# Kernel tuning notes

Measured on AMD Instinct MI355X. Metric: run time of the kernel, lower is better.

Reference implementation:

```python
import jax, jax.numpy as jnp
import numpy as np
from jax.scipy.special import logsumexp

B, T, D = 16, 512, 768
S, H, O = 4, 48, 48
EMISS_W = 0.5  # args.emiss_nn_weight


def setup_inputs() -> dict:
    key = jax.random.key(0)
    ks = jax.random.split(key, 6)
    emb = jax.random.normal(ks[0], (B, T, D), jnp.float32)
    # obs must be valid per-source distributions over n_obs (log is taken)
    obs = jax.nn.softmax(2.0 * jax.random.normal(ks[1], (B, T, S, O), jnp.float32), axis=-1)
    # default prior init: priors = 0.001, priors[0] = 1, param = log(priors)
    p = jnp.full((H,), 0.001, jnp.float32).at[0].set(1.0)
    state_priors = jnp.log(p)
    unnorm_trans = jax.random.normal(ks[2], (H, H), jnp.float32)
    unnorm_emiss = jnp.zeros((S, H, O), jnp.float32)
    # xavier_uniform with relu gain for the per-source emission Linears
    bound = np.sqrt(2.0) * np.sqrt(6.0 / (D + H * O))
    W_emiss = jax.random.uniform(ks[3], (S, H * O, D), jnp.float32, -bound, bound)
    b_emiss = jnp.zeros((S, H * O), jnp.float32)
    seq_lengths = jax.random.randint(ks[4], (B,), T // 2, T + 1).astype(jnp.int32)
    seq_lengths = seq_lengths.at[0].set(T)  # max length == T
    return dict(emb=emb, obs=obs, state_priors=state_priors, unnorm_trans=unnorm_trans,
                unnorm_emiss=unnorm_emiss, W_emiss=W_emiss, b_emiss=b_emiss,
                seq_lengths=seq_lengths)


def _lognorm(x):
    return x - logsumexp(x, axis=-1, keepdims=True)


def reference(emb, obs, state_priors, unnorm_trans, unnorm_emiss, W_emiss, b_emiss, seq_lengths):
    lp = jax.nn.log_softmax(state_priors)                 # [H]
    log_trans = jax.nn.log_softmax(unnorm_trans, axis=-1)  # [H,H] (constant over b,t)
    emiss = jax.nn.softmax(unnorm_emiss, axis=-1)          # [S,H,O]

    # neural emissions: per-source Linear(d_emb -> H*O), softmax over O
    logits = jnp.einsum('btd,sod->btso', emb, W_emiss) + b_emiss  # [B,T,S,H*O]
    nn_emiss = jax.nn.softmax(logits.reshape(B, T, S, H, O), axis=-1)
    # (nn_trans is computed by NeuralModule in the original but discarded)

    log_emiss = jnp.log((1.0 - EMISS_W) * emiss[None, None] + EMISS_W * nn_emiss)  # [B,T,S,H,O]
    # log_matmul over obs axis, then sum over sources -> [B,T,H]
    lep = logsumexp(log_emiss + jnp.log(obs)[:, :, :, None, :], axis=-1).sum(axis=2)

    # forward recursion (normalized each step)
    a0 = _lognorm(lp + lep[:, 0])                          # [B,H]

    def fstep(a_prev, lep_t):
        a = _lognorm(lep_t + logsumexp(a_prev[:, :, None] + log_trans[None], axis=1))
        return a, a

    _, alphas = jax.lax.scan(fstep, a0, jnp.swapaxes(lep[:, 1:], 0, 1))
    log_alpha = jnp.concatenate([a0[:, None], jnp.swapaxes(alphas, 0, 1)], axis=1)  # [B,T,H]

    # backward recursion: beta[t] = logsumexp_j(trans[i,j] + lep[t,j] + beta[t+1,j])
    bT = jnp.zeros((B, H), lep.dtype)

    def bstep(b_next, lep_t):
        b = logsumexp(log_trans[None] + (lep_t + b_next)[:, None, :], axis=2)
        return b, b

    _, betas = jax.lax.scan(bstep, bT, jnp.swapaxes(lep[:, :T - 1], 0, 1), reverse=True)
    log_beta = jnp.concatenate([jnp.swapaxes(betas, 0, 1), bT[:, None]], axis=1)  # [B,T,H]
    # per-example roll by (length - T) along time, as in the original
    log_beta = jax.vmap(lambda b, s: jnp.roll(b, s, axis=0))(log_beta, seq_lengths - T)

    log_gamma = _lognorm(log_alpha + log_beta)             # [B,T,H]

    # xi_t = trans + alpha[t-1] (outer-sum) (lep[t] + beta[t]),  t = 1..T-1
    xi = (log_trans[None, None]
          + log_alpha[:, :-1, :, None]
          + (lep[:, 1:] + log_beta[:, 1:])[:, :, None, :])  # [B,T-1,H,H]
    xi = xi - logsumexp(xi, axis=(-2, -1), keepdims=True)

    log_prior = jnp.mean(jnp.sum(jnp.exp(log_gamma[:, 0]) * lp, axis=-1))

    tran_terms = jnp.sum(jnp.exp(xi) * log_trans[None, None], axis=(-2, -1))  # [B,T-1]
    mask_tr = (jnp.arange(T - 1)[None] < (seq_lengths - 1)[:, None]).astype(lep.dtype)
    log_tran = jnp.mean(jnp.sum(tran_terms * mask_tr, axis=1))

    emis_terms = jnp.sum(jnp.exp(log_gamma) * lep, axis=-1)  # [B,T]
    mask_em = (jnp.arange(T)[None] < seq_lengths[:, None]).astype(lep.dtype)
    log_emis = jnp.mean(jnp.sum(emis_terms * mask_em, axis=1))

    return log_prior + log_tran + log_emis
```

## Files before the change

### kernel.cpp

```cpp
#include <hip/hip_runtime.h>
#include <math.h>

namespace {

constexpr int Bn = 16, Tn = 512, Dn = 768, Sn = 4, Hn = 48, On = 48;
constexpr int Mn = Bn * Tn;
constexpr int Gn = Sn * Hn;
constexpr int Nn = Gn * On;
constexpr float EMISS_W = 0.5f;

constexpr size_t OFF_LP   = 0;
constexpr size_t OFF_LT   = 64;
constexpr size_t OFF_PT   = OFF_LT + Hn*Hn;
constexpr size_t OFF_EM   = OFF_PT + Hn*Hn;
constexpr size_t OFF_LEPP = OFF_EM + (size_t)Sn*Hn*On;
constexpr size_t OFF_LA   = OFF_LEPP + (size_t)Mn*Gn;
constexpr size_t OFF_LB   = OFF_LA + (size_t)Mn*Hn;
constexpr size_t OFF_RED  = OFF_LB + (size_t)Mn*Hn;
constexpr size_t FLOATS_END = OFF_RED + (size_t)Mn;

typedef __attribute__((ext_vector_type(8))) short short8;
typedef __attribute__((ext_vector_type(4))) float f32x4;

__device__ inline float waveSum(float v){
#pragma unroll
  for (int o = 32; o; o >>= 1) v += __shfl_xor(v, o);
  return v;
}

__device__ inline unsigned short f2bf(float f){
  unsigned int u = __float_as_uint(f);
  u += 0x7FFFu + ((u >> 16) & 1u);
  return (unsigned short)(u >> 16);
}

__device__ inline void gload_lds16(const void* g, void* l){
  __builtin_amdgcn_global_load_lds(
      (const __attribute__((address_space(1))) void*)g,
      (__attribute__((address_space(3))) void*)l, 16, 0, 0);
}

__global__ void convprep_kernel(const float* __restrict__ srcA, unsigned short* __restrict__ dstA,
                                int n4a,
                                const float* __restrict__ srcB, unsigned short* __restrict__ dstB,
                                int n4b,
                                const float* __restrict__ sp, const float* __restrict__ ut,
                                const float* __restrict__ ue, float* __restrict__ ws,
                                int nconv){
  const int tid = threadIdx.x;
  if ((int)blockIdx.x == nconv){
    float m = -INFINITY;
    for (int h = 0; h < Hn; ++h) m = fmaxf(m, sp[h]);
    float s = 0.f;
    for (int h = 0; h < Hn; ++h) s += __expf(sp[h] - m);
    float lse = m + __logf(s);
    if (tid < Hn) ws[OFF_LP + tid] = sp[tid] - lse;
    if (tid < Hn){
      const float* row = ut + tid * Hn;
      float mm = -INFINITY;
      for (int j = 0; j < Hn; ++j) mm = fmaxf(mm, row[j]);
      float ss = 0.f;
      for (int j = 0; j < Hn; ++j) ss += __expf(row[j] - mm);
      float l = mm + __logf(ss);
      for (int j = 0; j < Hn; ++j){
        float v = row[j] - l;
        ws[OFF_LT + tid*Hn + j] = v;
        ws[OFF_PT + tid*Hn + j] = __expf(v);
      }
    }
    for (int r = tid; r < Sn*Hn; r += blockDim.x){
      const float* row = ue + (size_t)r * On;
      float mm = -INFINITY;
      for (int o = 0; o < On; ++o) mm = fmaxf(mm, row[o]);
      float ss = 0.f;
      for (int o = 0; o < On; ++o) ss += __expf(row[o] - mm);
      float inv = 1.f/ss;
      for (int o = 0; o < On; ++o) ws[OFF_EM + (size_t)r*On + o] = __expf(row[o]-mm)*inv;
    }
    return;
  }
  int i = blockIdx.x * blockDim.x + tid;
  const float* s2; unsigned short* d; int k;
  if (i < n4a){ s2 = srcA; d = dstA; k = i; }
  else { k = i - n4a; if (k >= n4b) return; s2 = srcB; d = dstB; }
  float4 v = ((const float4*)s2)[k];
  ushort4 r;
  r.x = f2bf(v.x); r.y = f2bf(v.y); r.z = f2bf(v.z); r.w = f2bf(v.w);
  ((ushort4*)d)[k] = r;
}

constexpr int MT = 128, NT2 = 96, KT = 64;

__global__ __launch_bounds__(256) void gemm_lep_kernel(
    const unsigned short* __restrict__ embB, const unsigned short* __restrict__ WB,
    const float* __restrict__ bm, const float* __restrict__ obs,
    float* __restrict__ ws){
  __shared__ __align__(16) char smem[128*97*4];
  __shared__ float bias_s[96], em_s[96];
  const int tid = threadIdx.x, lane = tid & 63, w = tid >> 6;
  const int m0 = blockIdx.x * MT;
  const int N0 = blockIdx.y * NT2;
  if (tid < 96){
    bias_s[tid] = bm[N0 + tid];
    em_s[tid]   = ws[OFF_EM + N0 + tid];
  }
  const int wm = w & 1, wn = w >> 1;
  const int lm = lane & 15, q = lane >> 4;
  const int key = lm & 7;
  const int srow = lane >> 3, spc = lane & 7;

  f32x4 acc[4][3];
#pragma unroll
  for (int i=0;i<4;++i)
#pragma unroll
    for (int j=0;j<3;++j) acc[i][j] = (f32x4){0.f,0.f,0.f,0.f};

  for (int kc = 0; kc < Dn; kc += KT){
    __syncthreads();
#pragma unroll
    for (int i=0;i<4;++i){
      int idx = w*4 + i;
      int row = idx*8 + srow;
      int lc  = spc ^ (row & 7);
      gload_lds16(embB + (size_t)(m0+row)*Dn + kc + lc*8, smem + idx*1024);
    }
#pragma unroll
    for (int i=0;i<3;++i){
      int idx = w*3 + i;
      int row = idx*8 + srow;
      int lc  = spc ^ (row & 7);
      gload_lds16(WB + (size_t)(N0+row)*Dn + kc + lc*8, smem + 16384 + idx*1024);
    }
    __syncthreads();
#pragma unroll
    for (int s = 0; s < 2; ++s){
      short8 af[4], bf[3];
#pragma unroll
      for (int i=0;i<4;++i){
        int row = wm*64 + i*16 + lm;
        af[i] = *(const short8*)(smem + row*128 + (((s*4+q) ^ key) * 16));
      }
#pragma unroll
      for (int j=0;j<3;++j){
        int row = wn*48 + j*16 + lm;
        bf[j] = *(const short8*)(smem + 16384 + row*128 + (((s*4+q) ^ key) * 16));
      }
#pragma unroll
      for (int i=0;i<4;++i)
#pragma unroll
        for (int j=0;j<3;++j)
          acc[i][j] = __builtin_amdgcn_mfma_f32_16x16x32_bf16(af[i], bf[j], acc[i][j], 0, 0, 0);
    }
  }
  __syncthreads();
  float* C = (float*)smem;
#pragma unroll
  for (int i=0;i<4;++i)
#pragma unroll
    for (int j=0;j<3;++j)
#pragma unroll
      for (int r=0;r<4;++r){
        int mrow = wm*64 + i*16 + q*4 + r;
        int ncol = wn*48 + j*16 + lm;
        C[mrow*97 + ncol] = acc[i][j][r];
      }
  __syncthreads();
  {
    const int row = tid >> 1, half = tid & 1;
    const int m = m0 + row;
    const int g = N0/48 + half;
    const int s2 = g / Hn;
    const float* crow = C + row*97 + half*48;
    const float* ob   = obs + ((size_t)m*Sn + s2)*On;
    const float* bi   = bias_s + half*48;
    const float* em   = em_s + half*48;
    float Z=0.f, pd=0.f, eo=0.f;
#pragma unroll
    for (int o=0;o<On;++o){
      float e = __expf(crow[o] + bi[o]);
      float obv = ob[o];
      Z += e;
      pd = fmaf(e, obv, pd);
      eo = fmaf(em[o], obv, eo);
    }
    float val = __logf((1.f-EMISS_W)*eo + EMISS_W*(pd/Z));
    ws[OFF_LEPP + (size_t)m*Gn + g] = val;
  }
}

constexpr int FBW = 24;
constexpr int FBL = 16;

__global__ __launch_bounds__(64) void fb_kernel(float* __restrict__ ws){
  __shared__ __align__(16) float ldsE[(FBW+FBL)*48];
  __shared__ __align__(16) float ring[2][64];
  const int lane = threadIdx.x;
  const int c    = blockIdx.x;
  const int b    = blockIdx.y;
  const bool fwd = blockIdx.z == 0;
  const bool act = lane < Hn;
  const int t0 = c*FBL, te = t0 + FBL - 1;

  float pt[Hn];
#pragma unroll
  for (int i = 0; i < Hn; ++i)
    pt[i] = act ? (fwd ? ws[OFF_PT + i*Hn + lane] : ws[OFF_PT + lane*Hn + i]) : 0.f;

  int row_lo, nrows, sA, sZ;
  bool exact;
  if (fwd){
    sA = t0 - FBW;
    exact = (sA < 1);
    row_lo = exact ? 0 : sA;
    if (exact) sA = 1;
    sZ = te;
    nrows = te - row_lo + 1;
  } else {
    int th = te + 1 + FBW;
    exact = (th > Tn - 2);
    sA = exact ? Tn - 2 : th - 1;
    sZ = t0;
    row_lo = t0;
    nrows = sA - t0 + 1;
  }

  {
    const float* src = ws + OFF_LEPP + ((size_t)b*Tn + row_lo)*Gn;
    int n4 = nrows * (Hn/4);
    for (int i = lane; i < n4; i += 64){
      int r = i / (Hn/4), h4 = i - r*(Hn/4);
      const float* p = src + (size_t)r*Gn + h4*4;
      float4 a = *(const float4*)(p);
      float4 b2 = *(const float4*)(p + Hn);
      float4 c2 = *(const float4*)(p + 2*Hn);
      float4 d2 = *(const float4*)(p + 3*Hn);
      float4 e;
      e.x = __expf(a.x + b2.x + c2.x + d2.x);
      e.y = __expf(a.y + b2.y + c2.y + d2.y);
      e.z = __expf(a.z + b2.z + c2.z + d2.z);
      e.w = __expf(a.w + b2.w + c2.w + d2.w);
      ((float4*)ldsE)[i] = e;
    }
  }
  __syncthreads();

  if (fwd){
    const size_t laF = OFF_LA + (size_t)b * Tn * Hn;
    float v;
    if (exact){
      v = act ? __expf(ws[OFF_LP + lane]) * ldsE[lane] : 0.f;
      if (c == 0 && act) ws[laF + lane] = v;
    } else {
      v = act ? 1.f : 0.f;
    }
    if (act) ring[0][lane] = v;
    __syncthreads();
    int cur = 0;
    for (int t = sA; t <= sZ; ++t){
      float S = waveSum(v);
      const float* rp = ring[cur];
      float s0=0.f,s1=0.f,s2=0.f,s3=0.f;
#pragma unroll
      for (int i = 0; i < Hn; i += 4){
        float4 a = *(const float4*)(rp + i);
        s0 = fmaf(a.x, pt[i+0], s0); s1 = fmaf(a.y, pt[i+1], s1);
        s2 = fmaf(a.z, pt[i+2], s2); s3 = fmaf(a.w, pt[i+3], s3);
      }
      float sd = (s0+s1)+(s2+s3);
      float e = act ? ldsE[(t - row_lo)*Hn + lane] : 0.f;
      float vn = act ? e * sd * (1.f/S) : 0.f;
      cur ^= 1;
      if (act) ring[cur][lane] = vn;
      __syncthreads();
      if (act && t >= t0) ws[laF + (size_t)t*Hn + lane] = vn;
      v = vn;
    }
  } else {
    const size_t lbF = OFF_LB + (size_t)b * Tn * Hn;
    float v = act ? 1.f : 0.f;
    if (exact && c == (Tn/FBL - 1) && act) ws[lbF + (size_t)(Tn-1)*Hn + lane] = 1.f;
    int cur = 0;
    for (int t = sA; t >= sZ; --t){
      float e = act ? ldsE[(t - row_lo)*Hn + lane] : 0.f;
      float wv = e * v;
      if (act) ring[cur][lane] = wv;
      float S = waveSum(wv);
      __syncthreads();
      const float* rp = ring[cur];
      float s0=0.f,s1=0.f,s2=0.f,s3=0.f;
#pragma unroll
      for (int j = 0; j < Hn; j += 4){
        float4 a = *(const float4*)(rp + j);
        s0 = fmaf(a.x, pt[j+0], s0); s1 = fmaf(a.y, pt[j+1], s1);
        s2 = fmaf(a.z, pt[j+2], s2); s3 = fmaf(a.w, pt[j+3], s3);
      }
      float vn = act ? ((s0+s1)+(s2+s3)) * (1.f/S) : 0.f;
      cur ^= 1;
      if (act && t <= te) ws[lbF + (size_t)t*Hn + lane] = vn;
      v = vn;
    }
  }
}

__global__ __launch_bounds__(256) void gamma_xi_kernel(
    const float* __restrict__ ws_c, float* __restrict__ ws,
    const int* __restrict__ seq_len){
  __shared__ float y_s[Hn], lap_s[Hn];
  __shared__ float red[8];
  const int tid = threadIdx.x;
  const int bid = blockIdx.x;
  const int b = bid >> 9, t = bid & (Tn-1);
  const int len = seq_len[b];
  int tb = t + (Tn - len); if (tb >= Tn) tb -= Tn;
  const size_t bt = (size_t)b*Tn + t;
  float lep = 0.f;
  if (tid < Hn){
    const float* lpp = ws_c + OFF_LEPP + bt*Gn + tid;
    lep = lpp[0] + lpp[Hn] + lpp[2*Hn] + lpp[3*Hn];
    float lb  = ws_c[OFF_LB + ((size_t)b*Tn + tb)*Hn + tid];
    y_s[tid] = __expf(lep) * lb;
    if (t >= 1) lap_s[tid] = ws_c[OFF_LA + (bt-1)*Hn + tid];
  }
  float emis_term = 0.f, prior_term = 0.f;
  if (tid < 64){
    int h = (tid < Hn) ? tid : 0;
    float la  = ws_c[OFF_LA + bt*Hn + h];
    float lb  = ws_c[OFF_LB + ((size_t)b*Tn + tb)*Hn + h];
    float lp  = ws_c[OFF_LP + h];
    float wgt = (tid < Hn) ? la*lb : 0.f;
    float Z = waveSum(wgt);
    float inv = 1.f / Z;
    emis_term  = waveSum(wgt * lep) * inv;
    prior_term = waveSum(wgt * lp) * inv;
  }
  __syncthreads();
  float tran_term = 0.f;
  if (t >= 1){
    float se = 0.f, st = 0.f;
#pragma unroll
    for (int k=0;k<9;++k){
      int e = tid + k*256;
      int i = e / Hn, j = e - i*Hn;
      float e2 = ws_c[OFF_PT + e] * lap_s[i] * y_s[j];
      se += e2;
      st = fmaf(e2, ws_c[OFF_LT + e], st);
    }
    se = waveSum(se);
    st = waveSum(st);
    const int wid = tid >> 6;
    if ((tid & 63) == 0){ red[wid] = se; red[4+wid] = st; }
    __syncthreads();
    if (tid == 0){
      float SE = red[0]+red[1]+red[2]+red[3];
      float ST = red[4]+red[5]+red[6]+red[7];
      tran_term = ST / SE;
    }
  }
  if (tid == 0){
    float tot = 0.f;
    if (t < len)            tot += emis_term;
    if (t == 0)             tot += prior_term;
    if (t >= 1 && t < len)  tot += tran_term;
    ws[OFF_RED + bid] = tot;
  }
}

__global__ __launch_bounds__(256) void sum_kernel(const float* __restrict__ ws,
                                                  float* __restrict__ out){
  __shared__ float red[4];
  const int tid = threadIdx.x;
  float s = 0.f;
  for (int i = tid; i < Mn; i += 256) s += ws[OFF_RED + i];
  s = waveSum(s);
  if ((tid & 63) == 0) red[tid >> 6] = s;
  __syncthreads();
  if (tid == 0) out[0] = (red[0]+red[1]+red[2]+red[3]) * (1.f / Bn);
}

}

extern "C" void kernel_launch(void* const* d_in, const int* in_sizes, int n_in,
                              void* d_out, int out_size, void* d_ws, size_t ws_size,
                              hipStream_t stream){
  const float* emb = (const float*)d_in[0];
  const float* obs = (const float*)d_in[1];
  const float* sp  = (const float*)d_in[2];
  const float* ut  = (const float*)d_in[3];
  const float* ue  = (const float*)d_in[4];
  const float* Wm  = (const float*)d_in[5];
  const float* bm  = (const float*)d_in[6];
  const int*   sl  = (const int*)d_in[7];
  float* ws  = (float*)d_ws;
  float* out = (float*)d_out;
  (void)in_sizes; (void)n_in; (void)ws_size; (void)out_size;

  unsigned short* embB = (unsigned short*)(ws + FLOATS_END);
  unsigned short* WB   = embB + (size_t)Mn * Dn;

  const int n4a = Mn*Dn/4, n4b = Nn*Dn/4;
  const int nconv = (n4a + n4b + 255)/256;
  convprep_kernel<<<nconv + 1, 256, 0, stream>>>(emb, embB, n4a, Wm, WB, n4b,
                                                 sp, ut, ue, ws, nconv);
  gemm_lep_kernel<<<dim3(Mn/MT, Nn/NT2), 256, 0, stream>>>(embB, WB, bm, obs, ws);
  fb_kernel<<<dim3(Tn/FBL, Bn, 2), 64, 0, stream>>>(ws);
  gamma_xi_kernel<<<Bn*Tn, 256, 0, stream>>>(ws, ws, sl);
  sum_kernel<<<1, 256, 0, stream>>>(ws, out);
}
```

Before: 293.4 us.

## Enlarge GEMM tiles, double-buffer LDS with interleaved prefetch, swizzle block order

The emission GEMM moves from 128x96 tiles with 256 threads to 256x192 tiles with 512 threads. It double-buffers the K slices in LDS, issuing next-slice global-to-LDS loads between the MFMA phases, and uses explicit barriers, waitcnt and setprio to overlap loads with compute. The block index is remapped so neighbouring blocks share operand tiles in cache. The epilogue runs in two halves through the reused LDS. Together these target GEMM memory latency and reuse, at the cost of higher register and LDS pressure, fewer blocks, and fragile hand-written synchronization.

```diff
diff --git a/kernel.cpp b/kernel.cpp
--- a/kernel.cpp
+++ b/kernel.cpp
@@ -89,18 +89,26 @@
   ((ushort4*)d)[k] = r;
 }
 
-constexpr int MT = 128, NT2 = 96, KT = 64;
-
-__global__ __launch_bounds__(256) void gemm_lep_kernel(
+constexpr int BM = 256, BN = 192, BK = 64;
+constexpr int NKT = Dn / BK;
+
+#define GEMM_BAR()  asm volatile("s_barrier" ::: "memory")
+#define GEMM_LGKM() do { asm volatile("s_waitcnt lgkmcnt(0)" ::: "memory"); \
+                         __builtin_amdgcn_sched_barrier(0); } while (0)
+
+__global__ __launch_bounds__(512, 2) void gemm_lep_kernel(
     const unsigned short* __restrict__ embB, const unsigned short* __restrict__ WB,
     const float* __restrict__ bm, const float* __restrict__ obs,
     float* __restrict__ ws){
-  __shared__ __align__(16) char smem[128*97*4];
-  __shared__ float bias_s[96], em_s[96];
+  __shared__ __align__(16) char smem[114688];
+  __shared__ float bias_s[192], em_s[192];
   const int tid = threadIdx.x, lane = tid & 63, w = tid >> 6;
-  const int m0 = blockIdx.x * MT;
-  const int N0 = blockIdx.y * NT2;
-  if (tid < 96){
+  const int bid = blockIdx.y * (Mn/BM) + blockIdx.x;
+  const int swz = (bid & 7) * 192 + (bid >> 3);
+  const int m0 = (swz & 31) * BM;
+  const int by = swz >> 5;
+  const int N0 = by * BN;
+  if (tid < 192){
     bias_s[tid] = bm[N0 + tid];
     em_s[tid]   = ws[OFF_EM + N0 + tid];
   }
@@ -108,83 +116,144 @@
   const int lm = lane & 15, q = lane >> 4;
   const int key = lm & 7;
   const int srow = lane >> 3, spc = lane & 7;
-
-  f32x4 acc[4][3];
-#pragma unroll
-  for (int i=0;i<4;++i)
-#pragma unroll
-    for (int j=0;j<3;++j) acc[i][j] = (f32x4){0.f,0.f,0.f,0.f};
-
-  for (int kc = 0; kc < Dn; kc += KT){
+  const int aoff0 = (q ^ key) << 4;
+  const int aoff1 = ((4 + q) ^ key) << 4;
+
+  f32x4 acc[8][3];
+#pragma unroll
+  for (int i = 0; i < 8; ++i)
+#pragma unroll
+    for (int j = 0; j < 3; ++j) acc[i][j] = (f32x4){0.f,0.f,0.f,0.f};
+
+  auto stageA = [&](int kt, int i){
+    const int idx = w*4 + i;
+    const int row = idx*8 + srow;
+    const int lc  = spc ^ (row & 7);
+    gload_lds16(embB + (size_t)(m0+row)*Dn + kt*BK + lc*8,
+                smem + ((kt & 1) << 15) + idx*1024);
+  };
+  auto stageB = [&](int kt, int i){
+    const int idx = w*3 + i;
+    const int row = idx*8 + srow;
+    const int lc  = spc ^ (row & 7);
+    gload_lds16(WB + (size_t)(N0+row)*Dn + kt*BK + lc*8,
+                smem + 65536 + (kt & 1)*24576 + idx*1024);
+  };
+
+#pragma unroll
+  for (int i = 0; i < 4; ++i) stageA(0, i);
+#pragma unroll
+  for (int i = 0; i < 3; ++i) stageB(0, i);
+  asm volatile("s_waitcnt vmcnt(0)" ::: "memory");
+  GEMM_BAR();
+
+  for (int kt = 0; kt < NKT; ++kt){
+    const char* Ab = smem + ((kt & 1) << 15);
+    const char* Bb = smem + 65536 + (kt & 1)*24576;
+    const int pf = kt + 1;
+    const bool dopf = pf < NKT;
+    short8 af[4], bf[3];
+
+#pragma unroll
+    for (int j = 0; j < 3; ++j)
+      bf[j] = *(const short8*)(Bb + (wn*48 + j*16 + lm)*128 + aoff0);
+#pragma unroll
+    for (int i = 0; i < 4; ++i)
+      af[i] = *(const short8*)(Ab + (wm*128 + i*16 + lm)*128 + aoff0);
+    if (dopf){ stageA(pf, 0); stageA(pf, 1); stageB(pf, 0); }
+    GEMM_BAR(); GEMM_LGKM();
+    __builtin_amdgcn_s_setprio(1);
+#pragma unroll
+    for (int i = 0; i < 4; ++i)
+#pragma unroll
+      for (int j = 0; j < 3; ++j)
+        acc[i][j] = __builtin_amdgcn_mfma_f32_16x16x32_bf16(af[i], bf[j], acc[i][j], 0, 0, 0);
+    __builtin_amdgcn_s_setprio(0);
+    GEMM_BAR();
+
+#pragma unroll
+    for (int i = 0; i < 4; ++i)
+      af[i] = *(const short8*)(Ab + (wm*128 + (4+i)*16 + lm)*128 + aoff0);
+    if (dopf){ stageA(pf, 2); stageA(pf, 3); stageB(pf, 1); }
+    GEMM_BAR(); GEMM_LGKM();
+    __builtin_amdgcn_s_setprio(1);
+#pragma unroll
+    for (int i = 0; i < 4; ++i)
+#pragma unroll
+      for (int j = 0; j < 3; ++j)
+        acc[4+i][j] = __builtin_amdgcn_mfma_f32_16x16x32_bf16(af[i], bf[j], acc[4+i][j], 0, 0, 0);
+    __builtin_amdgcn_s_setprio(0);
+    GEMM_BAR();
+
+#pragma unroll
+    for (int j = 0; j < 3; ++j)
+      bf[j] = *(const short8*)(Bb + (wn*48 + j*16 + lm)*128 + aoff1);
+#pragma unroll
+    for (int i = 0; i < 4; ++i)
+      af[i] = *(const short8*)(Ab + (wm*128 + i*16 + lm)*128 + aoff1);
+    if (dopf){ stageB(pf, 2); }
+    GEMM_BAR(); GEMM_LGKM();
+    __builtin_amdgcn_s_setprio(1);
+#pragma unroll
+    for (int i = 0; i < 4; ++i)
+#pragma unroll
+      for (int j = 0; j < 3; ++j)
+        acc[i][j] = __builtin_amdgcn_mfma_f32_16x16x32_bf16(af[i], bf[j], acc[i][j], 0, 0, 0);
+    __builtin_amdgcn_s_setprio(0);
+    GEMM_BAR();
+
+#pragma unroll
+    for (int i = 0; i < 4; ++i)
+      af[i] = *(const short8*)(Ab + (wm*128 + (4+i)*16 + lm)*128 + aoff1);
+    GEMM_BAR(); GEMM_LGKM();
+    __builtin_amdgcn_s_setprio(1);
+#pragma unroll
+    for (int i = 0; i < 4; ++i)
+#pragma unroll
+      for (int j = 0; j < 3; ++j)
+        acc[4+i][j] = __builtin_amdgcn_mfma_f32_16x16x32_bf16(af[i], bf[j], acc[4+i][j], 0, 0, 0);
+    __builtin_amdgcn_s_setprio(0);
+    asm volatile("s_waitcnt vmcnt(0)" ::: "memory");
+    GEMM_BAR();
+  }
+
+  float* Cp = (float*)smem;
+#pragma unroll
+  for (int h = 0; h < 2; ++h){
+    if (h) __syncthreads();
+#pragma unroll
+    for (int i = 0; i < 4; ++i)
+#pragma unroll
+      for (int j = 0; j < 3; ++j){
+        const int col = wn*48 + j*16 + lm;
+#pragma unroll
+        for (int r = 0; r < 4; ++r){
+          const int rowl = wm*64 + i*16 + q*4 + r;
+          Cp[rowl*193 + col] = acc[h*4+i][j][r];
+        }
+      }
     __syncthreads();
-#pragma unroll
-    for (int i=0;i<4;++i){
-      int idx = w*4 + i;
-      int row = idx*8 + srow;
-      int lc  = spc ^ (row & 7);
-      gload_lds16(embB + (size_t)(m0+row)*Dn + kc + lc*8, smem + idx*1024);
-    }
-#pragma unroll
-    for (int i=0;i<3;++i){
-      int idx = w*3 + i;
-      int row = idx*8 + srow;
-      int lc  = spc ^ (row & 7);
-      gload_lds16(WB + (size_t)(N0+row)*Dn + kc + lc*8, smem + 16384 + idx*1024);
-    }
-    __syncthreads();
-#pragma unroll
-    for (int s = 0; s < 2; ++s){
-      short8 af[4], bf[3];
-#pragma unroll
-      for (int i=0;i<4;++i){
-        int row = wm*64 + i*16 + lm;
-        af[i] = *(const short8*)(smem + row*128 + (((s*4+q) ^ key) * 16));
+    {
+      const int rowl = tid >> 2, grp = tid & 3;
+      const int trow = (rowl >> 6)*128 + h*64 + (rowl & 63);
+      const int m = m0 + trow;
+      const int g = by*4 + grp;
+      const int s2 = g / Hn;
+      const float* crow = Cp + rowl*193 + grp*48;
+      const float* ob   = obs + ((size_t)m*Sn + s2)*On;
+      const float* bi   = bias_s + grp*48;
+      const float* em   = em_s + grp*48;
+      float Z = 0.f, pd = 0.f, eo = 0.f;
+#pragma unroll
+      for (int o = 0; o < On; ++o){
+        float e = __expf(crow[o] + bi[o]);
+        float obv = ob[o];
+        Z += e;
+        pd = fmaf(e, obv, pd);
+        eo = fmaf(em[o], obv, eo);
       }
-#pragma unroll
-      for (int j=0;j<3;++j){
-        int row = wn*48 + j*16 + lm;
-        bf[j] = *(const short8*)(smem + 16384 + row*128 + (((s*4+q) ^ key) * 16));
-      }
-#pragma unroll
-      for (int i=0;i<4;++i)
-#pragma unroll
-        for (int j=0;j<3;++j)
-          acc[i][j] = __builtin_amdgcn_mfma_f32_16x16x32_bf16(af[i], bf[j], acc[i][j], 0, 0, 0);
-    }
-  }
-  __syncthreads();
-  float* C = (float*)smem;
-#pragma unroll
-  for (int i=0;i<4;++i)
-#pragma unroll
-    for (int j=0;j<3;++j)
-#pragma unroll
-      for (int r=0;r<4;++r){
-        int mrow = wm*64 + i*16 + q*4 + r;
-        int ncol = wn*48 + j*16 + lm;
-        C[mrow*97 + ncol] = acc[i][j][r];
-      }
-  __syncthreads();
-  {
-    const int row = tid >> 1, half = tid & 1;
-    const int m = m0 + row;
-    const int g = N0/48 + half;
-    const int s2 = g / Hn;
-    const float* crow = C + row*97 + half*48;
-    const float* ob   = obs + ((size_t)m*Sn + s2)*On;
-    const float* bi   = bias_s + half*48;
-    const float* em   = em_s + half*48;
-    float Z=0.f, pd=0.f, eo=0.f;
-#pragma unroll
-    for (int o=0;o<On;++o){
-      float e = __expf(crow[o] + bi[o]);
-      float obv = ob[o];
-      Z += e;
-      pd = fmaf(e, obv, pd);
-      eo = fmaf(em[o], obv, eo);
-    }
-    float val = __logf((1.f-EMISS_W)*eo + EMISS_W*(pd/Z));
-    ws[OFF_LEPP + (size_t)m*Gn + g] = val;
+      ws[OFF_LEPP + (size_t)m*Gn + g] = __logf((1.f-EMISS_W)*eo + EMISS_W*(pd/Z));
+    }
   }
 }
 
@@ -401,7 +470,7 @@
   const int nconv = (n4a + n4b + 255)/256;
   convprep_kernel<<<nconv + 1, 256, 0, stream>>>(emb, embB, n4a, Wm, WB, n4b,
                                                  sp, ut, ue, ws, nconv);
-  gemm_lep_kernel<<<dim3(Mn/MT, Nn/NT2), 256, 0, stream>>>(embB, WB, bm, obs, ws);
+  gemm_lep_kernel<<<dim3(Mn/BM, Nn/BN), 512, 0, stream>>>(embB, WB, bm, obs, ws);
   fb_kernel<<<dim3(Tn/FBL, Bn, 2), 64, 0, stream>>>(ws);
   gamma_xi_kernel<<<Bn*Tn, 256, 0, stream>>>(ws, ws, sl);
   sum_kernel<<<1, 256, 0, stream>>>(ws, out);
```

New measurement: 313.2 us. 1.07x slower.
